# Kernel tuning notes

Measured on AMD Instinct MI355X. Metric: run time of the kernel, lower is better.

Reference implementation:

```python
import jax, jax.numpy as jnp
import numpy as np

N_NODES = 65536
N_EDGES = 1048576
D_IN = 1024
D_HID = 64
N_CLS = 32


def gcn_conv(x, W, b, src, dst, n_nodes):
    """PyG GCNConv: linear transform, then symmetric-normalized aggregation
    with implicit self-loops (fill value 1)."""
    xw = x @ W  # [N, d_out]
    e = src.shape[0]
    # degree over destination index, including the self-loop (+1)
    deg = jax.ops.segment_sum(jnp.ones((e,), xw.dtype), dst, num_segments=n_nodes) + 1.0
    dinv_sqrt = jax.lax.rsqrt(deg)  # deg >= 1, safe
    norm = dinv_sqrt[src] * dinv_sqrt[dst]  # [E]
    agg = jax.ops.segment_sum(xw[src] * norm[:, None], dst, num_segments=n_nodes)
    # self-loop contribution: norm = deg_i^{-1}
    agg = agg + xw * (1.0 / deg)[:, None]
    return agg + b


def setup_inputs() -> dict:
    key = jax.random.key(0)
    k_x, k_e, k_w1, k_b1, k_w2, k_b2 = jax.random.split(key, 6)
    x = jax.random.normal(k_x, (N_NODES, D_IN), dtype=jnp.float32)
    edge_index = jax.random.randint(k_e, (2, N_EDGES), 0, N_NODES, dtype=jnp.int64)
    s1 = 1.0 / np.sqrt(D_IN)
    s2 = 1.0 / np.sqrt(D_HID)
    W1 = jax.random.uniform(k_w1, (D_IN, D_HID), jnp.float32, -s1, s1)
    b1 = jax.random.uniform(k_b1, (D_HID,), jnp.float32, -s1, s1)
    W2 = jax.random.uniform(k_w2, (D_HID, N_CLS), jnp.float32, -s2, s2)
    b2 = jax.random.uniform(k_b2, (N_CLS,), jnp.float32, -s2, s2)
    return {"x": x, "edge_index": edge_index, "W1": W1, "b1": b1, "W2": W2, "b2": b2}


def reference(x, edge_index, W1, b1, W2, b2):
    src, dst = edge_index[0], edge_index[1]
    n = x.shape[0]
    h = gcn_conv(x, W1, b1, src, dst, n)
    h = jax.nn.relu(h)
    # dropout is identity in eval mode
    h = gcn_conv(h, W2, b2, src, dst, n)
    return jax.nn.log_softmax(h, axis=1)
```

## Files before the change

### kernel.cpp

```cpp
#include <hip/hip_runtime.h>
#include <hip/hip_bf16.h>

#define N_NODES 65536
#define D_IN 1024
#define D_HID 64
#define N_CLS 32
#define NBUK 256
#define NSB 256

typedef short short8 __attribute__((ext_vector_type(8)));
typedef float floatx4 __attribute__((ext_vector_type(4)));

__device__ __forceinline__ unsigned short f2bf(float f) {
  union { float f; unsigned u; } cv; cv.f = f;
  unsigned r = (cv.u + 0x7FFFu + ((cv.u >> 16) & 1u)) >> 16;
  return (unsigned short)r;
}
__device__ __forceinline__ float2 bf2f2(unsigned v) {
  union { unsigned u; float f; } a, b;
  a.u = v << 16;
  b.u = v & 0xFFFF0000u;
  return make_float2(a.f, b.f);
}

__global__ void k_hist_w1t(const int* __restrict__ dst, int* __restrict__ H,
                           const float* __restrict__ w1, unsigned short* __restrict__ w1t,
                           int e4) {
  int b = blockIdx.x, t = threadIdx.x;
  if (b >= NSB) {
    int i = (b - NSB) * 256 + t;
    int k = i / D_HID, n = i % D_HID;
    w1t[n * D_IN + k] = f2bf(w1[i]);
    return;
  }
  __shared__ int hist[NBUK];
  hist[t] = 0;
  __syncthreads();
  const int4* d4 = (const int4*)dst + b * 1024;
#pragma unroll
  for (int p = 0; p < 4; p++) {
    int i4 = b * 1024 + p * 256 + t;
    if (i4 < e4) {
      int4 d = d4[p * 256 + t];
      atomicAdd(&hist[d.x >> 8], 1);
      atomicAdd(&hist[d.y >> 8], 1);
      atomicAdd(&hist[d.z >> 8], 1);
      atomicAdd(&hist[d.w >> 8], 1);
    }
  }
  __syncthreads();
  H[b * NBUK + t] = hist[t];
}

__global__ void k_scan_bin(const int* __restrict__ H, int* __restrict__ Hs,
                           int* __restrict__ btot) {
  int bin = blockIdx.x, t = threadIdx.x;
  int v = H[t * NBUK + bin];
  __shared__ int s[256];
  s[t] = v;
  __syncthreads();
  for (int off = 1; off < 256; off <<= 1) {
    int x = (t >= off) ? s[t - off] : 0;
    __syncthreads();
    s[t] += x;
    __syncthreads();
  }
  Hs[bin * NSB + t] = s[t] - v;
  if (t == 255) btot[bin] = s[255];
}

__global__ void k_scan_tot(const int* __restrict__ btot, int* __restrict__ btoff,
                           int* __restrict__ rowptr, int e) {
  __shared__ int s[256];
  int t = threadIdx.x;
  int v = btot[t];
  s[t] = v;
  __syncthreads();
  for (int off = 1; off < 256; off <<= 1) {
    int x = (t >= off) ? s[t - off] : 0;
    __syncthreads();
    s[t] += x;
    __syncthreads();
  }
  btoff[t] = s[t] - v;
  if (t == 0) rowptr[N_NODES] = e;
}

__global__ __launch_bounds__(256) void k_scatter_gemm1(
    const int* __restrict__ dst, const int* __restrict__ src,
    const int* __restrict__ Hs, const int* __restrict__ btoff,
    unsigned* __restrict__ pk, int e4,
    const float* __restrict__ x, const unsigned short* __restrict__ w1t,
    unsigned short* __restrict__ xw1s) {
  if (blockIdx.x < NSB) {
    __shared__ int cnt[NBUK], sc[NBUK], cur[NBUK], base2[NBUK];
    __shared__ unsigned stage[4096];
    int b = blockIdx.x, t = threadIdx.x;
    cnt[t] = 0;
    __syncthreads();
    const int4* d4 = (const int4*)dst + b * 1024;
    const int4* s4 = (const int4*)src + b * 1024;
    int4 dv[4], sv[4]; bool ok[4];
#pragma unroll
    for (int p = 0; p < 4; p++) {
      int i4 = b * 1024 + p * 256 + t;
      ok[p] = i4 < e4;
      if (ok[p]) {
        dv[p] = d4[p * 256 + t];
        sv[p] = s4[p * 256 + t];
        atomicAdd(&cnt[dv[p].x >> 8], 1);
        atomicAdd(&cnt[dv[p].y >> 8], 1);
        atomicAdd(&cnt[dv[p].z >> 8], 1);
        atomicAdd(&cnt[dv[p].w >> 8], 1);
      }
    }
    __syncthreads();
    int c = cnt[t];
    sc[t] = c;
    __syncthreads();
    for (int off = 1; off < 256; off <<= 1) {
      int xv = (t >= off) ? sc[t - off] : 0;
      __syncthreads();
      sc[t] += xv;
      __syncthreads();
    }
    int excl = sc[t] - c;
    cur[t] = excl;
    base2[t] = btoff[t] + Hs[t * NSB + b] - excl;
    __syncthreads();
    int tot = sc[255];
#pragma unroll
    for (int p = 0; p < 4; p++) {
      if (ok[p]) {
        int d[4] = {dv[p].x, dv[p].y, dv[p].z, dv[p].w};
        int s[4] = {sv[p].x, sv[p].y, sv[p].z, sv[p].w};
#pragma unroll
        for (int j = 0; j < 4; j++) {
          int pos = atomicAdd(&cur[d[j] >> 8], 1);
          stage[pos] = ((unsigned)d[j] << 16) | (unsigned)s[j];
        }
      }
    }
    __syncthreads();
    for (int i = t; i < tot; i += 256) {
      unsigned u = stage[i];
      pk[base2[u >> 24] + i] = u;
    }
    return;
  }
  int wave = threadIdx.x >> 6;
  int lane = threadIdx.x & 63;
  int quad = lane >> 4;
  int l16 = lane & 15;
  int rowbase = (blockIdx.x - NSB) * 64 + wave * 16;
  const float* xrow = x + (size_t)(rowbase + l16) * D_IN + quad * 8;
  const unsigned short* bbase = w1t + quad * 8;
  floatx4 acc[4];
#pragma unroll
  for (int nt = 0; nt < 4; nt++) acc[nt] = (floatx4){0.f, 0.f, 0.f, 0.f};
  float4 p0 = *(const float4*)(xrow + 0);
  float4 p1 = *(const float4*)(xrow + 4);
  float4 p2 = *(const float4*)(xrow + 32);
  float4 p3 = *(const float4*)(xrow + 36);
  short8 bf0[4], bf1[4];
#pragma unroll
  for (int nt = 0; nt < 4; nt++) {
    const unsigned short* bp = bbase + (size_t)(nt * 16 + l16) * D_IN;
    bf0[nt] = *(const short8*)(bp);
    bf1[nt] = *(const short8*)(bp + 32);
  }
  for (int k0 = 0; k0 < D_IN; k0 += 64) {
    float4 c0 = p0, c1 = p1, c2 = p2, c3 = p3;
    int kn = (k0 + 64 < D_IN) ? k0 + 64 : k0;
    p0 = *(const float4*)(xrow + kn);
    p1 = *(const float4*)(xrow + kn + 4);
    p2 = *(const float4*)(xrow + kn + 32);
    p3 = *(const float4*)(xrow + kn + 36);
    float av0[8] = {c0.x, c0.y, c0.z, c0.w, c1.x, c1.y, c1.z, c1.w};
    float av1[8] = {c2.x, c2.y, c2.z, c2.w, c3.x, c3.y, c3.z, c3.w};
    short8 af0, af1;
    unsigned* u0 = (unsigned*)&af0;
    unsigned* u1 = (unsigned*)&af1;
#pragma unroll
    for (int j = 0; j < 4; j++) {
      asm("v_cvt_pk_bf16_f32 %0, %1, %2" : "=v"(u0[j]) : "v"(av0[2 * j]), "v"(av0[2 * j + 1]));
      asm("v_cvt_pk_bf16_f32 %0, %1, %2" : "=v"(u1[j]) : "v"(av1[2 * j]), "v"(av1[2 * j + 1]));
    }
#pragma unroll
    for (int nt = 0; nt < 4; nt++)
      acc[nt] = __builtin_amdgcn_mfma_f32_16x16x32_bf16(af0, bf0[nt], acc[nt], 0, 0, 0);
#pragma unroll
    for (int nt = 0; nt < 4; nt++)
      bf0[nt] = *(const short8*)(bbase + (size_t)(nt * 16 + l16) * D_IN + kn);
#pragma unroll
    for (int nt = 0; nt < 4; nt++)
      acc[nt] = __builtin_amdgcn_mfma_f32_16x16x32_bf16(af1, bf1[nt], acc[nt], 0, 0, 0);
#pragma unroll
    for (int nt = 0; nt < 4; nt++)
      bf1[nt] = *(const short8*)(bbase + (size_t)(nt * 16 + l16) * D_IN + kn + 32);
  }
#pragma unroll
  for (int r = 0; r < 4; r++) {
    int row = rowbase + quad * 4 + r;
#pragma unroll
    for (int nt = 0; nt < 4; nt++)
      xw1s[(size_t)row * D_HID + nt * 16 + l16] = f2bf(acc[nt][r]);
  }
}

__global__ void k_bucket_csr(const unsigned* __restrict__ pk, const int* __restrict__ btoff,
                             const int* __restrict__ btot, int* __restrict__ rowptr,
                             int* __restrict__ csr_src, float* __restrict__ dinv) {
  __shared__ int cnt[NBUK], sc[NBUK], cur[NBUK];
  int bin = blockIdx.x, t = threadIdx.x;
  cnt[t] = 0;
  __syncthreads();
  int beg = btoff[bin], len = btot[bin];
  for (int i = t; i < len; i += 256)
    atomicAdd(&cnt[(pk[beg + i] >> 16) & 255], 1);
  __syncthreads();
  int c = cnt[t];
  sc[t] = c;
  __syncthreads();
  for (int off = 1; off < 256; off <<= 1) {
    int x = (t >= off) ? sc[t - off] : 0;
    __syncthreads();
    sc[t] += x;
    __syncthreads();
  }
  int excl = sc[t] - c;
  int node = bin * 256 + t;
  rowptr[node] = beg + excl;
  dinv[node] = rsqrtf((float)(c + 1));
  cur[t] = excl;
  __syncthreads();
  for (int i = t; i < len; i += 256) {
    unsigned u = pk[beg + i];
    int p = atomicAdd(&cur[(u >> 16) & 255], 1);
    csr_src[beg + p] = (int)(u & 0xFFFFu);
  }
}

__global__ __launch_bounds__(256) void k_agg1(const unsigned* __restrict__ xw1s2,
    const int* __restrict__ rowptr, const int* __restrict__ csr_src,
    const float* __restrict__ dinv, const float* __restrict__ b1,
    const float* __restrict__ w2, unsigned short* __restrict__ xw2s) {
  __shared__ float w2s[D_HID * N_CLS];
  for (int i = threadIdx.x; i < D_HID * N_CLS; i += 256) w2s[i] = w2[i];
  __syncthreads();
  int wave = threadIdx.x >> 6;
  int lane = threadIdx.x & 63;
  int h = lane >> 5, l = lane & 31;
  int node = blockIdx.x * 4 + wave;
  float dd = dinv[node];
  int beg = rowptr[node], end = rowptr[node + 1];
  float cx[8], cy[8];
#pragma unroll
  for (int j = 0; j < 8; j++) { cx[j] = 0.f; cy[j] = 0.f; }
  for (int e = beg + h; e < end; e += 16) {
    int idx[8]; bool val[8];
#pragma unroll
    for (int j = 0; j < 8; j++) {
      int ee = e + 2 * j;
      val[j] = ee < end;
      idx[j] = csr_src[val[j] ? ee : beg];
    }
    float dv[8];
#pragma unroll
    for (int j = 0; j < 8; j++) dv[j] = dinv[idx[j]];
#pragma unroll
    for (int j = 0; j < 8; j++) {
      float2 v = bf2f2(xw1s2[(size_t)idx[j] * 32 + l]);
      float w = val[j] ? dv[j] : 0.f;
      cx[j] += w * v.x;
      cy[j] += w * v.y;
    }
  }
  float sx = ((cx[0] + cx[1]) + (cx[2] + cx[3])) + ((cx[4] + cx[5]) + (cx[6] + cx[7]));
  float sy = ((cy[0] + cy[1]) + (cy[2] + cy[3])) + ((cy[4] + cy[5]) + (cy[6] + cy[7]));
  sx += __shfl_xor(sx, 32);
  sy += __shfl_xor(sy, 32);
  float2 self = bf2f2(xw1s2[(size_t)node * 32 + l]);
  float2 bb = ((const float2*)b1)[l];
  float vx = dd * (sx + dd * self.x) + bb.x;
  float vy = dd * (sy + dd * self.y) + bb.y;
  vx = vx > 0.f ? vx : 0.f;
  vy = vy > 0.f ? vy : 0.f;
  int c = lane & 31;
  float p = 0.f;
#pragma unroll
  for (int kk = 0; kk < 32; kk++) {
    int k = h * 32 + kk;
    float hv = (k & 1) ? __shfl(vy, k >> 1) : __shfl(vx, k >> 1);
    p += hv * w2s[k * N_CLS + c];
  }
  p += __shfl_xor(p, 32);
  if (lane < 32) xw2s[(size_t)node * N_CLS + c] = f2bf(p * dd);
}

__global__ __launch_bounds__(256) void k_agg2(const unsigned* __restrict__ xw2s2,
    const int* __restrict__ rowptr, const int* __restrict__ csr_src,
    const float* __restrict__ dinv, const float* __restrict__ b2,
    float* __restrict__ out) {
  int wave = threadIdx.x >> 6;
  int lane = threadIdx.x & 63;
  int q = lane >> 4, l = lane & 15;
  int node = blockIdx.x * 4 + wave;
  float dd = dinv[node];
  int beg = rowptr[node], end = rowptr[node + 1];
  float cx[4], cy[4];
#pragma unroll
  for (int j = 0; j < 4; j++) { cx[j] = 0.f; cy[j] = 0.f; }
  for (int e = beg + q; e < end; e += 16) {
    int idx[4]; bool val[4];
#pragma unroll
    for (int j = 0; j < 4; j++) {
      int ee = e + 4 * j;
      val[j] = ee < end;
      idx[j] = csr_src[val[j] ? ee : beg];
    }
#pragma unroll
    for (int j = 0; j < 4; j++) {
      float2 v = bf2f2(xw2s2[(size_t)idx[j] * 16 + l]);
      cx[j] += val[j] ? v.x : 0.f;
      cy[j] += val[j] ? v.y : 0.f;
    }
  }
  float sx = (cx[0] + cx[1]) + (cx[2] + cx[3]);
  float sy = (cy[0] + cy[1]) + (cy[2] + cy[3]);
  sx += __shfl_xor(sx, 32); sy += __shfl_xor(sy, 32);
  sx += __shfl_xor(sx, 16); sy += __shfl_xor(sy, 16);
  float2 self = bf2f2(xw2s2[(size_t)node * 16 + l]);
  float2 bb = ((const float2*)b2)[l];
  float lx = dd * (sx + self.x) + bb.x;
  float ly = dd * (sy + self.y) + bb.y;
  float m = fmaxf(lx, ly);
#pragma unroll
  for (int o = 8; o > 0; o >>= 1) m = fmaxf(m, __shfl_xor(m, o));
  float s2 = __expf(lx - m) + __expf(ly - m);
#pragma unroll
  for (int o = 8; o > 0; o >>= 1) s2 += __shfl_xor(s2, o);
  float lse = m + __logf(s2);
  if (lane < 16)
    ((float2*)out)[(size_t)node * 16 + l] = make_float2(lx - lse, ly - lse);
}

extern "C" void kernel_launch(void* const* d_in, const int* in_sizes, int n_in,
                              void* d_out, int out_size, void* d_ws, size_t ws_size,
                              hipStream_t stream) {
  (void)n_in; (void)out_size; (void)ws_size;
  const float* x  = (const float*)d_in[0];
  const int*   ei = (const int*)d_in[1];
  const float* w1 = (const float*)d_in[2];
  const float* b1 = (const float*)d_in[3];
  const float* w2 = (const float*)d_in[4];
  const float* b2 = (const float*)d_in[5];
  float* out = (float*)d_out;
  int e = in_sizes[1] / 2;
  const int* src = ei;
  const int* dst = ei + e;

  char* ws = (char*)d_ws;
  int* H              = (int*)(ws + 0x0000000);
  int* Hs             = (int*)(ws + 0x0040000);
  int* btot           = (int*)(ws + 0x0080000);
  int* btoff          = (int*)(ws + 0x0080400);
  int* rowptr         = (int*)(ws + 0x0081000);
  float* dinv         = (float*)(ws + 0x00D0000);
  unsigned* pk        = (unsigned*)(ws + 0x0200000);
  int* csr_src        = (int*)(ws + 0x0600000);
  unsigned short* w1t = (unsigned short*)(ws + 0x0A00000);
  unsigned short* xw1s= (unsigned short*)(ws + 0x0A20000);
  unsigned short* xw2s= (unsigned short*)(ws + 0x1220000);

  int e4 = e / 4;
  k_hist_w1t    <<<NSB + 256, 256, 0, stream>>>(dst, H, w1, w1t, e4);
  k_scan_bin    <<<NBUK, 256, 0, stream>>>(H, Hs, btot);
  k_scan_tot    <<<1, 256, 0, stream>>>(btot, btoff, rowptr, e);
  k_scatter_gemm1<<<NSB + 1024, 256, 0, stream>>>(dst, src, Hs, btoff, pk, e4,
                                                  x, w1t, xw1s);
  k_bucket_csr  <<<NBUK, 256, 0, stream>>>(pk, btoff, btot, rowptr, csr_src, dinv);
  k_agg1        <<<N_NODES / 4, 256, 0, stream>>>((const unsigned*)xw1s, rowptr, csr_src,
                                                  dinv, b1, w2, xw2s);
  k_agg2        <<<N_NODES / 4, 256, 0, stream>>>((const unsigned*)xw2s, rowptr, csr_src,
                                                  dinv, b2, out);
}
```

Before: 489.5 us.

## Spread GEMM1 row tiles across all CSR-build kernels to overlap work

The layer-1 GEMM (1024 row tiles) used to run only inside the scatter kernel. It is now split into chunks of 384, 128, 128, 256 and 128 tiles, piggybacked as extra blocks on the histogram, two scan kernels, scatter and bucket-CSR kernels. This fills the otherwise underused GPU during the small serial CSR stages with compute-heavy GEMM work. It costs an extra small launch for the W1 transpose and puts GEMM register pressure into every kernel, which may lower occupancy for the CSR blocks.

After: 553.1 us. 13.0% more time.

```diff
diff --git a/kernel.cpp b/kernel.cpp
--- a/kernel.cpp
+++ b/kernel.cpp
@@ -23,136 +23,14 @@
   return make_float2(a.f, b.f);
 }
 
-__global__ void k_hist_w1t(const int* __restrict__ dst, int* __restrict__ H,
-                           const float* __restrict__ w1, unsigned short* __restrict__ w1t,
-                           int e4) {
-  int b = blockIdx.x, t = threadIdx.x;
-  if (b >= NSB) {
-    int i = (b - NSB) * 256 + t;
-    int k = i / D_HID, n = i % D_HID;
-    w1t[n * D_IN + k] = f2bf(w1[i]);
-    return;
-  }
-  __shared__ int hist[NBUK];
-  hist[t] = 0;
-  __syncthreads();
-  const int4* d4 = (const int4*)dst + b * 1024;
-#pragma unroll
-  for (int p = 0; p < 4; p++) {
-    int i4 = b * 1024 + p * 256 + t;
-    if (i4 < e4) {
-      int4 d = d4[p * 256 + t];
-      atomicAdd(&hist[d.x >> 8], 1);
-      atomicAdd(&hist[d.y >> 8], 1);
-      atomicAdd(&hist[d.z >> 8], 1);
-      atomicAdd(&hist[d.w >> 8], 1);
-    }
-  }
-  __syncthreads();
-  H[b * NBUK + t] = hist[t];
-}
-
-__global__ void k_scan_bin(const int* __restrict__ H, int* __restrict__ Hs,
-                           int* __restrict__ btot) {
-  int bin = blockIdx.x, t = threadIdx.x;
-  int v = H[t * NBUK + bin];
-  __shared__ int s[256];
-  s[t] = v;
-  __syncthreads();
-  for (int off = 1; off < 256; off <<= 1) {
-    int x = (t >= off) ? s[t - off] : 0;
-    __syncthreads();
-    s[t] += x;
-    __syncthreads();
-  }
-  Hs[bin * NSB + t] = s[t] - v;
-  if (t == 255) btot[bin] = s[255];
-}
-
-__global__ void k_scan_tot(const int* __restrict__ btot, int* __restrict__ btoff,
-                           int* __restrict__ rowptr, int e) {
-  __shared__ int s[256];
-  int t = threadIdx.x;
-  int v = btot[t];
-  s[t] = v;
-  __syncthreads();
-  for (int off = 1; off < 256; off <<= 1) {
-    int x = (t >= off) ? s[t - off] : 0;
-    __syncthreads();
-    s[t] += x;
-    __syncthreads();
-  }
-  btoff[t] = s[t] - v;
-  if (t == 0) rowptr[N_NODES] = e;
-}
-
-__global__ __launch_bounds__(256) void k_scatter_gemm1(
-    const int* __restrict__ dst, const int* __restrict__ src,
-    const int* __restrict__ Hs, const int* __restrict__ btoff,
-    unsigned* __restrict__ pk, int e4,
-    const float* __restrict__ x, const unsigned short* __restrict__ w1t,
-    unsigned short* __restrict__ xw1s) {
-  if (blockIdx.x < NSB) {
-    __shared__ int cnt[NBUK], sc[NBUK], cur[NBUK], base2[NBUK];
-    __shared__ unsigned stage[4096];
-    int b = blockIdx.x, t = threadIdx.x;
-    cnt[t] = 0;
-    __syncthreads();
-    const int4* d4 = (const int4*)dst + b * 1024;
-    const int4* s4 = (const int4*)src + b * 1024;
-    int4 dv[4], sv[4]; bool ok[4];
-#pragma unroll
-    for (int p = 0; p < 4; p++) {
-      int i4 = b * 1024 + p * 256 + t;
-      ok[p] = i4 < e4;
-      if (ok[p]) {
-        dv[p] = d4[p * 256 + t];
-        sv[p] = s4[p * 256 + t];
-        atomicAdd(&cnt[dv[p].x >> 8], 1);
-        atomicAdd(&cnt[dv[p].y >> 8], 1);
-        atomicAdd(&cnt[dv[p].z >> 8], 1);
-        atomicAdd(&cnt[dv[p].w >> 8], 1);
-      }
-    }
-    __syncthreads();
-    int c = cnt[t];
-    sc[t] = c;
-    __syncthreads();
-    for (int off = 1; off < 256; off <<= 1) {
-      int xv = (t >= off) ? sc[t - off] : 0;
-      __syncthreads();
-      sc[t] += xv;
-      __syncthreads();
-    }
-    int excl = sc[t] - c;
-    cur[t] = excl;
-    base2[t] = btoff[t] + Hs[t * NSB + b] - excl;
-    __syncthreads();
-    int tot = sc[255];
-#pragma unroll
-    for (int p = 0; p < 4; p++) {
-      if (ok[p]) {
-        int d[4] = {dv[p].x, dv[p].y, dv[p].z, dv[p].w};
-        int s[4] = {sv[p].x, sv[p].y, sv[p].z, sv[p].w};
-#pragma unroll
-        for (int j = 0; j < 4; j++) {
-          int pos = atomicAdd(&cur[d[j] >> 8], 1);
-          stage[pos] = ((unsigned)d[j] << 16) | (unsigned)s[j];
-        }
-      }
-    }
-    __syncthreads();
-    for (int i = t; i < tot; i += 256) {
-      unsigned u = stage[i];
-      pk[base2[u >> 24] + i] = u;
-    }
-    return;
-  }
-  int wave = threadIdx.x >> 6;
-  int lane = threadIdx.x & 63;
+__device__ __forceinline__ void gemm1_body(int rb, int tid,
+    const float* __restrict__ x, const unsigned short* __restrict__ w1t,
+    unsigned short* __restrict__ xw1s) {
+  int wave = tid >> 6;
+  int lane = tid & 63;
   int quad = lane >> 4;
   int l16 = lane & 15;
-  int rowbase = (blockIdx.x - NSB) * 64 + wave * 16;
+  int rowbase = rb * 64 + wave * 16;
   const float* xrow = x + (size_t)(rowbase + l16) * D_IN + quad * 8;
   const unsigned short* bbase = w1t + quad * 8;
   floatx4 acc[4];
@@ -208,11 +86,147 @@
   }
 }
 
-__global__ void k_bucket_csr(const unsigned* __restrict__ pk, const int* __restrict__ btoff,
-                             const int* __restrict__ btot, int* __restrict__ rowptr,
-                             int* __restrict__ csr_src, float* __restrict__ dinv) {
+__global__ void k_w1t(const float* __restrict__ w1, unsigned short* __restrict__ w1t) {
+  int i = blockIdx.x * 256 + threadIdx.x;
+  int k = i / D_HID, n = i % D_HID;
+  w1t[n * D_IN + k] = f2bf(w1[i]);
+}
+
+__global__ __launch_bounds__(256) void k_hist_g(const int* __restrict__ dst,
+    int* __restrict__ H, int e4,
+    const float* __restrict__ x, const unsigned short* __restrict__ w1t,
+    unsigned short* __restrict__ xw1s) {
+  int b = blockIdx.x, t = threadIdx.x;
+  if (b >= NSB) { gemm1_body(b - NSB, t, x, w1t, xw1s); return; }
+  __shared__ int hist[NBUK];
+  hist[t] = 0;
+  __syncthreads();
+  const int4* d4 = (const int4*)dst + b * 1024;
+#pragma unroll
+  for (int p = 0; p < 4; p++) {
+    int i4 = b * 1024 + p * 256 + t;
+    if (i4 < e4) {
+      int4 d = d4[p * 256 + t];
+      atomicAdd(&hist[d.x >> 8], 1);
+      atomicAdd(&hist[d.y >> 8], 1);
+      atomicAdd(&hist[d.z >> 8], 1);
+      atomicAdd(&hist[d.w >> 8], 1);
+    }
+  }
+  __syncthreads();
+  H[b * NBUK + t] = hist[t];
+}
+
+__global__ __launch_bounds__(256) void k_scanbin_g(const int* __restrict__ H,
+    int* __restrict__ Hs, int* __restrict__ btot,
+    const float* __restrict__ x, const unsigned short* __restrict__ w1t,
+    unsigned short* __restrict__ xw1s) {
+  int bin = blockIdx.x, t = threadIdx.x;
+  if (bin >= NBUK) { gemm1_body(384 + bin - NBUK, t, x, w1t, xw1s); return; }
+  int v = H[t * NBUK + bin];
+  __shared__ int s[256];
+  s[t] = v;
+  __syncthreads();
+  for (int off = 1; off < 256; off <<= 1) {
+    int xv = (t >= off) ? s[t - off] : 0;
+    __syncthreads();
+    s[t] += xv;
+    __syncthreads();
+  }
+  Hs[bin * NSB + t] = s[t] - v;
+  if (t == 255) btot[bin] = s[255];
+}
+
+__global__ __launch_bounds__(256) void k_scantot_g(const int* __restrict__ btot,
+    int* __restrict__ btoff, int* __restrict__ rowptr, int e,
+    const float* __restrict__ x, const unsigned short* __restrict__ w1t,
+    unsigned short* __restrict__ xw1s) {
+  int t = threadIdx.x;
+  if (blockIdx.x >= 1) { gemm1_body(512 + (int)blockIdx.x - 1, t, x, w1t, xw1s); return; }
+  __shared__ int s[256];
+  int v = btot[t];
+  s[t] = v;
+  __syncthreads();
+  for (int off = 1; off < 256; off <<= 1) {
+    int xv = (t >= off) ? s[t - off] : 0;
+    __syncthreads();
+    s[t] += xv;
+    __syncthreads();
+  }
+  btoff[t] = s[t] - v;
+  if (t == 0) rowptr[N_NODES] = e;
+}
+
+__global__ __launch_bounds__(256) void k_scatter_g(
+    const int* __restrict__ dst, const int* __restrict__ src,
+    const int* __restrict__ Hs, const int* __restrict__ btoff,
+    unsigned* __restrict__ pk, int e4,
+    const float* __restrict__ x, const unsigned short* __restrict__ w1t,
+    unsigned short* __restrict__ xw1s) {
+  int b = blockIdx.x, t = threadIdx.x;
+  if (b >= NSB) { gemm1_body(640 + b - NSB, t, x, w1t, xw1s); return; }
+  __shared__ int cnt[NBUK], sc[NBUK], cur[NBUK], base2[NBUK];
+  __shared__ unsigned stage[4096];
+  cnt[t] = 0;
+  __syncthreads();
+  const int4* d4 = (const int4*)dst + b * 1024;
+  const int4* s4 = (const int4*)src + b * 1024;
+  int4 dv[4], sv[4]; bool ok[4];
+#pragma unroll
+  for (int p = 0; p < 4; p++) {
+    int i4 = b * 1024 + p * 256 + t;
+    ok[p] = i4 < e4;
+    if (ok[p]) {
+      dv[p] = d4[p * 256 + t];
+      sv[p] = s4[p * 256 + t];
+      atomicAdd(&cnt[dv[p].x >> 8], 1);
+      atomicAdd(&cnt[dv[p].y >> 8], 1);
+      atomicAdd(&cnt[dv[p].z >> 8], 1);
+      atomicAdd(&cnt[dv[p].w >> 8], 1);
+    }
+  }
+  __syncthreads();
+  int c = cnt[t];
+  sc[t] = c;
+  __syncthreads();
+  for (int off = 1; off < 256; off <<= 1) {
+    int xv = (t >= off) ? sc[t - off] : 0;
+    __syncthreads();
+    sc[t] += xv;
+    __syncthreads();
+  }
+  int excl = sc[t] - c;
+  cur[t] = excl;
+  base2[t] = btoff[t] + Hs[t * NSB + b] - excl;
+  __syncthreads();
+  int tot = sc[255];
+#pragma unroll
+  for (int p = 0; p < 4; p++) {
+    if (ok[p]) {
+      int d[4] = {dv[p].x, dv[p].y, dv[p].z, dv[p].w};
+      int s[4] = {sv[p].x, sv[p].y, sv[p].z, sv[p].w};
+#pragma unroll
+      for (int j = 0; j < 4; j++) {
+        int pos = atomicAdd(&cur[d[j] >> 8], 1);
+        stage[pos] = ((unsigned)d[j] << 16) | (unsigned)s[j];
+      }
+    }
+  }
+  __syncthreads();
+  for (int i = t; i < tot; i += 256) {
+    unsigned u = stage[i];
+    pk[base2[u >> 24] + i] = u;
+  }
+}
+
+__global__ __launch_bounds__(256) void k_bucketcsr_g(const unsigned* __restrict__ pk,
+    const int* __restrict__ btoff, const int* __restrict__ btot,
+    int* __restrict__ rowptr, int* __restrict__ csr_src, float* __restrict__ dinv,
+    const float* __restrict__ x, const unsigned short* __restrict__ w1t,
+    unsigned short* __restrict__ xw1s) {
+  int bin = blockIdx.x, t = threadIdx.x;
+  if (bin >= NBUK) { gemm1_body(896 + bin - NBUK, t, x, w1t, xw1s); return; }
   __shared__ int cnt[NBUK], sc[NBUK], cur[NBUK];
-  int bin = blockIdx.x, t = threadIdx.x;
   cnt[t] = 0;
   __syncthreads();
   int beg = btoff[bin], len = btot[bin];
@@ -223,9 +237,9 @@
   sc[t] = c;
   __syncthreads();
   for (int off = 1; off < 256; off <<= 1) {
-    int x = (t >= off) ? sc[t - off] : 0;
-    __syncthreads();
-    sc[t] += x;
+    int x2 = (t >= off) ? sc[t - off] : 0;
+    __syncthreads();
+    sc[t] += x2;
     __syncthreads();
   }
   int excl = sc[t] - c;
@@ -374,14 +388,15 @@
   unsigned short* xw2s= (unsigned short*)(ws + 0x1220000);
 
   int e4 = e / 4;
-  k_hist_w1t    <<<NSB + 256, 256, 0, stream>>>(dst, H, w1, w1t, e4);
-  k_scan_bin    <<<NBUK, 256, 0, stream>>>(H, Hs, btot);
-  k_scan_tot    <<<1, 256, 0, stream>>>(btot, btoff, rowptr, e);
-  k_scatter_gemm1<<<NSB + 1024, 256, 0, stream>>>(dst, src, Hs, btoff, pk, e4,
-                                                  x, w1t, xw1s);
-  k_bucket_csr  <<<NBUK, 256, 0, stream>>>(pk, btoff, btot, rowptr, csr_src, dinv);
-  k_agg1        <<<N_NODES / 4, 256, 0, stream>>>((const unsigned*)xw1s, rowptr, csr_src,
-                                                  dinv, b1, w2, xw2s);
-  k_agg2        <<<N_NODES / 4, 256, 0, stream>>>((const unsigned*)xw2s, rowptr, csr_src,
-                                                  dinv, b2, out);
-}
+  k_w1t       <<<256, 256, 0, stream>>>(w1, w1t);
+  k_hist_g    <<<NSB + 384, 256, 0, stream>>>(dst, H, e4, x, w1t, xw1s);
+  k_scanbin_g <<<NBUK + 128, 256, 0, stream>>>(H, Hs, btot, x, w1t, xw1s);
+  k_scantot_g <<<1 + 128, 256, 0, stream>>>(btot, btoff, rowptr, e, x, w1t, xw1s);
+  k_scatter_g <<<NSB + 256, 256, 0, stream>>>(dst, src, Hs, btoff, pk, e4, x, w1t, xw1s);
+  k_bucketcsr_g<<<NBUK + 128, 256, 0, stream>>>(pk, btoff, btot, rowptr, csr_src, dinv,
+                                                x, w1t, xw1s);
+  k_agg1      <<<N_NODES / 4, 256, 0, stream>>>((const unsigned*)xw1s, rowptr, csr_src,
+                                                dinv, b1, w2, xw2s);
+  k_agg2      <<<N_NODES / 4, 256, 0, stream>>>((const unsigned*)xw2s, rowptr, csr_src,
+                                                dinv, b2, out);
+}
```

## Aggregate per destination bucket with LDS atomics instead of building CSR

Applied to the files above, without the earlier changes.

Drops the per-node CSR build (rowptr and csr_src) and aggregates straight from the bucketed packed edges. Each block handles one 256-node bucket and accumulates into a shared-memory buffer with float atomics, then applies self-loop, bias, ReLU and the W2 projection (layer 1) or log-softmax (layer 2). This removes the CSR scatter pass and the per-node indirection. In exchange it uses only 256 blocks, LDS atomic contention, a large shared-memory footprint that limits occupancy, and a nondeterministic summation order.

New measurement: 940.1 us. +92.0%, slower.

```diff
diff --git a/kernel.cpp b/kernel.cpp
--- a/kernel.cpp
+++ b/kernel.cpp
@@ -69,8 +69,7 @@
   if (t == 255) btot[bin] = s[255];
 }
 
-__global__ void k_scan_tot(const int* __restrict__ btot, int* __restrict__ btoff,
-                           int* __restrict__ rowptr, int e) {
+__global__ void k_scan_tot(const int* __restrict__ btot, int* __restrict__ btoff) {
   __shared__ int s[256];
   int t = threadIdx.x;
   int v = btot[t];
@@ -83,7 +82,6 @@
     __syncthreads();
   }
   btoff[t] = s[t] - v;
-  if (t == 0) rowptr[N_NODES] = e;
 }
 
 __global__ __launch_bounds__(256) void k_scatter_gemm1(
@@ -208,10 +206,9 @@
   }
 }
 
-__global__ void k_bucket_csr(const unsigned* __restrict__ pk, const int* __restrict__ btoff,
-                             const int* __restrict__ btot, int* __restrict__ rowptr,
-                             int* __restrict__ csr_src, float* __restrict__ dinv) {
-  __shared__ int cnt[NBUK], sc[NBUK], cur[NBUK];
+__global__ void k_deg(const unsigned* __restrict__ pk, const int* __restrict__ btoff,
+                      const int* __restrict__ btot, float* __restrict__ dinv) {
+  __shared__ int cnt[NBUK];
   int bin = blockIdx.x, t = threadIdx.x;
   cnt[t] = 0;
   __syncthreads();
@@ -219,130 +216,114 @@
   for (int i = t; i < len; i += 256)
     atomicAdd(&cnt[(pk[beg + i] >> 16) & 255], 1);
   __syncthreads();
-  int c = cnt[t];
-  sc[t] = c;
-  __syncthreads();
-  for (int off = 1; off < 256; off <<= 1) {
-    int x = (t >= off) ? sc[t - off] : 0;
-    __syncthreads();
-    sc[t] += x;
-    __syncthreads();
-  }
-  int excl = sc[t] - c;
-  int node = bin * 256 + t;
-  rowptr[node] = beg + excl;
-  dinv[node] = rsqrtf((float)(c + 1));
-  cur[t] = excl;
-  __syncthreads();
-  for (int i = t; i < len; i += 256) {
-    unsigned u = pk[beg + i];
-    int p = atomicAdd(&cur[(u >> 16) & 255], 1);
-    csr_src[beg + p] = (int)(u & 0xFFFFu);
-  }
-}
-
-__global__ __launch_bounds__(256) void k_agg1(const unsigned* __restrict__ xw1s2,
-    const int* __restrict__ rowptr, const int* __restrict__ csr_src,
-    const float* __restrict__ dinv, const float* __restrict__ b1,
-    const float* __restrict__ w2, unsigned short* __restrict__ xw2s) {
+  dinv[bin * 256 + t] = rsqrtf((float)(cnt[t] + 1));
+}
+
+__global__ __launch_bounds__(512) void k_agg1b(const unsigned* __restrict__ pk,
+    const int* __restrict__ btoff, const int* __restrict__ btot,
+    const unsigned* __restrict__ xw1s2, const float* __restrict__ dinv,
+    const float* __restrict__ b1, const float* __restrict__ w2,
+    unsigned short* __restrict__ xw2s) {
+  __shared__ float hbuf[256][64];
   __shared__ float w2s[D_HID * N_CLS];
-  for (int i = threadIdx.x; i < D_HID * N_CLS; i += 256) w2s[i] = w2[i];
-  __syncthreads();
-  int wave = threadIdx.x >> 6;
-  int lane = threadIdx.x & 63;
-  int h = lane >> 5, l = lane & 31;
-  int node = blockIdx.x * 4 + wave;
-  float dd = dinv[node];
-  int beg = rowptr[node], end = rowptr[node + 1];
-  float cx[8], cy[8];
-#pragma unroll
-  for (int j = 0; j < 8; j++) { cx[j] = 0.f; cy[j] = 0.f; }
-  for (int e = beg + h; e < end; e += 16) {
-    int idx[8]; bool val[8];
+  int t = threadIdx.x, bin = blockIdx.x;
+  for (int i = t; i < D_HID * N_CLS; i += 512) w2s[i] = w2[i];
+  for (int i = t; i < 256 * 64; i += 512) ((float*)hbuf)[i] = 0.f;
+  __syncthreads();
+  int beg = btoff[bin], len = btot[bin];
+  int hw = t >> 5;
+  int l = t & 31;
+  for (int e0 = hw * 8; e0 < len; e0 += 128) {
+    unsigned u[8]; bool ok[8];
 #pragma unroll
     for (int j = 0; j < 8; j++) {
-      int ee = e + 2 * j;
-      val[j] = ee < end;
-      idx[j] = csr_src[val[j] ? ee : beg];
+      int e = e0 + j;
+      ok[j] = e < len;
+      u[j] = pk[beg + (ok[j] ? e : 0)];
     }
     float dv[8];
 #pragma unroll
-    for (int j = 0; j < 8; j++) dv[j] = dinv[idx[j]];
+    for (int j = 0; j < 8; j++) dv[j] = dinv[u[j] & 0xFFFFu];
 #pragma unroll
     for (int j = 0; j < 8; j++) {
-      float2 v = bf2f2(xw1s2[(size_t)idx[j] * 32 + l]);
-      float w = val[j] ? dv[j] : 0.f;
-      cx[j] += w * v.x;
-      cy[j] += w * v.y;
-    }
-  }
-  float sx = ((cx[0] + cx[1]) + (cx[2] + cx[3])) + ((cx[4] + cx[5]) + (cx[6] + cx[7]));
-  float sy = ((cy[0] + cy[1]) + (cy[2] + cy[3])) + ((cy[4] + cy[5]) + (cy[6] + cy[7]));
-  sx += __shfl_xor(sx, 32);
-  sy += __shfl_xor(sy, 32);
-  float2 self = bf2f2(xw1s2[(size_t)node * 32 + l]);
-  float2 bb = ((const float2*)b1)[l];
-  float vx = dd * (sx + dd * self.x) + bb.x;
-  float vy = dd * (sy + dd * self.y) + bb.y;
-  vx = vx > 0.f ? vx : 0.f;
-  vy = vy > 0.f ? vy : 0.f;
-  int c = lane & 31;
-  float p = 0.f;
-#pragma unroll
-  for (int kk = 0; kk < 32; kk++) {
-    int k = h * 32 + kk;
-    float hv = (k & 1) ? __shfl(vy, k >> 1) : __shfl(vx, k >> 1);
-    p += hv * w2s[k * N_CLS + c];
-  }
-  p += __shfl_xor(p, 32);
-  if (lane < 32) xw2s[(size_t)node * N_CLS + c] = f2bf(p * dd);
-}
-
-__global__ __launch_bounds__(256) void k_agg2(const unsigned* __restrict__ xw2s2,
-    const int* __restrict__ rowptr, const int* __restrict__ csr_src,
-    const float* __restrict__ dinv, const float* __restrict__ b2,
-    float* __restrict__ out) {
-  int wave = threadIdx.x >> 6;
-  int lane = threadIdx.x & 63;
-  int q = lane >> 4, l = lane & 15;
-  int node = blockIdx.x * 4 + wave;
-  float dd = dinv[node];
-  int beg = rowptr[node], end = rowptr[node + 1];
-  float cx[4], cy[4];
-#pragma unroll
-  for (int j = 0; j < 4; j++) { cx[j] = 0.f; cy[j] = 0.f; }
-  for (int e = beg + q; e < end; e += 16) {
-    int idx[4]; bool val[4];
-#pragma unroll
-    for (int j = 0; j < 4; j++) {
-      int ee = e + 4 * j;
-      val[j] = ee < end;
-      idx[j] = csr_src[val[j] ? ee : beg];
-    }
-#pragma unroll
-    for (int j = 0; j < 4; j++) {
-      float2 v = bf2f2(xw2s2[(size_t)idx[j] * 16 + l]);
-      cx[j] += val[j] ? v.x : 0.f;
-      cy[j] += val[j] ? v.y : 0.f;
-    }
-  }
-  float sx = (cx[0] + cx[1]) + (cx[2] + cx[3]);
-  float sy = (cy[0] + cy[1]) + (cy[2] + cy[3]);
-  sx += __shfl_xor(sx, 32); sy += __shfl_xor(sy, 32);
-  sx += __shfl_xor(sx, 16); sy += __shfl_xor(sy, 16);
-  float2 self = bf2f2(xw2s2[(size_t)node * 16 + l]);
-  float2 bb = ((const float2*)b2)[l];
-  float lx = dd * (sx + self.x) + bb.x;
-  float ly = dd * (sy + self.y) + bb.y;
-  float m = fmaxf(lx, ly);
-#pragma unroll
-  for (int o = 8; o > 0; o >>= 1) m = fmaxf(m, __shfl_xor(m, o));
-  float s2 = __expf(lx - m) + __expf(ly - m);
-#pragma unroll
-  for (int o = 8; o > 0; o >>= 1) s2 += __shfl_xor(s2, o);
-  float lse = m + __logf(s2);
-  if (lane < 16)
-    ((float2*)out)[(size_t)node * 16 + l] = make_float2(lx - lse, ly - lse);
+      float2 v = bf2f2(xw1s2[(size_t)(u[j] & 0xFFFFu) * 32 + l]);
+      if (ok[j]) {
+        int d = (u[j] >> 16) & 255;
+        atomicAdd(&hbuf[d][2 * l], dv[j] * v.x);
+        atomicAdd(&hbuf[d][2 * l + 1], dv[j] * v.y);
+      }
+    }
+  }
+  __syncthreads();
+  for (int i = t; i < 256 * 32; i += 512) {
+    int n = i >> 5, ll = i & 31;
+    int node = bin * 256 + n;
+    float dd = dinv[node];
+    float2 self = bf2f2(xw1s2[(size_t)node * 32 + ll]);
+    float2 bb = ((const float2*)b1)[ll];
+    float hx = dd * (hbuf[n][2 * ll] + dd * self.x) + bb.x;
+    float hy = dd * (hbuf[n][2 * ll + 1] + dd * self.y) + bb.y;
+    hbuf[n][2 * ll] = hx > 0.f ? hx : 0.f;
+    hbuf[n][2 * ll + 1] = hy > 0.f ? hy : 0.f;
+  }
+  __syncthreads();
+  for (int i = t; i < 256 * 32; i += 512) {
+    int n = i >> 5, c = i & 31;
+    int node = bin * 256 + n;
+    float p = 0.f;
+#pragma unroll
+    for (int k = 0; k < 64; k++) p += hbuf[n][k] * w2s[k * N_CLS + c];
+    xw2s[(size_t)node * N_CLS + c] = f2bf(p * dinv[node]);
+  }
+}
+
+__global__ __launch_bounds__(512) void k_agg2b(const unsigned* __restrict__ pk,
+    const int* __restrict__ btoff, const int* __restrict__ btot,
+    const unsigned* __restrict__ xw2s2, const float* __restrict__ dinv,
+    const float* __restrict__ b2, float* __restrict__ out) {
+  __shared__ float obuf[256][32];
+  int t = threadIdx.x, bin = blockIdx.x;
+  for (int i = t; i < 256 * 32; i += 512) ((float*)obuf)[i] = 0.f;
+  __syncthreads();
+  int beg = btoff[bin], len = btot[bin];
+  int qw = t >> 4;
+  int l = t & 15;
+  for (int e0 = qw * 8; e0 < len; e0 += 256) {
+    unsigned u[8]; bool ok[8];
+#pragma unroll
+    for (int j = 0; j < 8; j++) {
+      int e = e0 + j;
+      ok[j] = e < len;
+      u[j] = pk[beg + (ok[j] ? e : 0)];
+    }
+#pragma unroll
+    for (int j = 0; j < 8; j++) {
+      float2 v = bf2f2(xw2s2[(size_t)(u[j] & 0xFFFFu) * 16 + l]);
+      if (ok[j]) {
+        int d = (u[j] >> 16) & 255;
+        atomicAdd(&obuf[d][2 * l], v.x);
+        atomicAdd(&obuf[d][2 * l + 1], v.y);
+      }
+    }
+  }
+  __syncthreads();
+  for (int i = t; i < 256 * 16; i += 512) {
+    int n = i >> 4, ll = i & 15;
+    int node = bin * 256 + n;
+    float dd = dinv[node];
+    float2 self = bf2f2(xw2s2[(size_t)node * 16 + ll]);
+    float2 bb = ((const float2*)b2)[ll];
+    float lx = dd * (obuf[n][2 * ll] + self.x) + bb.x;
+    float ly = dd * (obuf[n][2 * ll + 1] + self.y) + bb.y;
+    float m = fmaxf(lx, ly);
+#pragma unroll
+    for (int o = 8; o > 0; o >>= 1) m = fmaxf(m, __shfl_xor(m, o));
+    float s2 = __expf(lx - m) + __expf(ly - m);
+#pragma unroll
+    for (int o = 8; o > 0; o >>= 1) s2 += __shfl_xor(s2, o);
+    float lse = m + __logf(s2);
+    ((float2*)out)[(size_t)node * 16 + ll] = make_float2(lx - lse, ly - lse);
+  }
 }
 
 extern "C" void kernel_launch(void* const* d_in, const int* in_sizes, int n_in,
@@ -365,23 +346,21 @@
   int* Hs             = (int*)(ws + 0x0040000);
   int* btot           = (int*)(ws + 0x0080000);
   int* btoff          = (int*)(ws + 0x0080400);
-  int* rowptr         = (int*)(ws + 0x0081000);
   float* dinv         = (float*)(ws + 0x00D0000);
   unsigned* pk        = (unsigned*)(ws + 0x0200000);
-  int* csr_src        = (int*)(ws + 0x0600000);
   unsigned short* w1t = (unsigned short*)(ws + 0x0A00000);
   unsigned short* xw1s= (unsigned short*)(ws + 0x0A20000);
   unsigned short* xw2s= (unsigned short*)(ws + 0x1220000);
 
   int e4 = e / 4;
-  k_hist_w1t    <<<NSB + 256, 256, 0, stream>>>(dst, H, w1, w1t, e4);
-  k_scan_bin    <<<NBUK, 256, 0, stream>>>(H, Hs, btot);
-  k_scan_tot    <<<1, 256, 0, stream>>>(btot, btoff, rowptr, e);
+  k_hist_w1t     <<<NSB + 256, 256, 0, stream>>>(dst, H, w1, w1t, e4);
+  k_scan_bin     <<<NBUK, 256, 0, stream>>>(H, Hs, btot);
+  k_scan_tot     <<<1, 256, 0, stream>>>(btot, btoff);
   k_scatter_gemm1<<<NSB + 1024, 256, 0, stream>>>(dst, src, Hs, btoff, pk, e4,
                                                   x, w1t, xw1s);
-  k_bucket_csr  <<<NBUK, 256, 0, stream>>>(pk, btoff, btot, rowptr, csr_src, dinv);
-  k_agg1        <<<N_NODES / 4, 256, 0, stream>>>((const unsigned*)xw1s, rowptr, csr_src,
-                                                  dinv, b1, w2, xw2s);
-  k_agg2        <<<N_NODES / 4, 256, 0, stream>>>((const unsigned*)xw2s, rowptr, csr_src,
-                                                  dinv, b2, out);
-}
+  k_deg          <<<NBUK, 256, 0, stream>>>(pk, btoff, btot, dinv);
+  k_agg1b        <<<NBUK, 512, 0, stream>>>(pk, btoff, btot, (const unsigned*)xw1s,
+                                            dinv, b1, w2, xw2s);
+  k_agg2b        <<<NBUK, 512, 0, stream>>>(pk, btoff, btot, (const unsigned*)xw2s,
+                                            dinv, b2, out);
+}
```
